# Optimization experiments

Measured on AMD Instinct MI355X. Metric: run time of the kernel, lower is better.

The kernel has to match this reference:

```python
import jax, jax.numpy as jnp
import numpy as np

B, S, D = 1, 4096, 512
QK_DIM, N_HEADS = 512, 8
HEAD_DIM = QK_DIM // N_HEADS


def setup_inputs() -> dict:
    key = jax.random.key(0)
    ks = jax.random.split(key, 9)
    s_in = 1.0 / np.sqrt(D)
    s_v = 1.0 / np.sqrt(QK_DIM)
    return {
        "x": jax.random.normal(ks[0], (B, S, D), dtype=jnp.float32),
        # torch nn.Linear convention: weight (out_features, in_features)
        "Wq": jax.random.uniform(ks[1], (QK_DIM, D), jnp.float32, -s_in, s_in),
        "bq": jax.random.uniform(ks[2], (QK_DIM,), jnp.float32, -s_in, s_in),
        "Wk": jax.random.uniform(ks[3], (QK_DIM, D), jnp.float32, -s_in, s_in),
        "bk": jax.random.uniform(ks[4], (QK_DIM,), jnp.float32, -s_in, s_in),
        "Wv": jax.random.uniform(ks[5], (QK_DIM, D), jnp.float32, -s_in, s_in),
        "bv": jax.random.uniform(ks[6], (QK_DIM,), jnp.float32, -s_in, s_in),
        "Wo": jax.random.uniform(ks[7], (D, QK_DIM), jnp.float32, -s_v, s_v),
        "bo": jax.random.uniform(ks[8], (D,), jnp.float32, -s_v, s_v),
    }


def reference(x, Wq, bq, Wk, bk, Wv, bv, Wo, bo):
    # Faithful to source: tokens flattened over batch*seq before head split.
    n = x.shape[0] * x.shape[1]  # B*S
    Q = (x @ Wq.T + bq).reshape(n, N_HEADS, HEAD_DIM).transpose(1, 0, 2)  # (H, N, hd)
    K = (x @ Wk.T + bk).reshape(n, N_HEADS, HEAD_DIM).transpose(1, 0, 2)
    V = (x @ Wv.T + bv).reshape(n, N_HEADS, HEAD_DIM).transpose(1, 0, 2)
    scores = jnp.einsum("hnd,hmd->hnm", Q, K) / np.sqrt(HEAD_DIM).astype(np.float32)
    attn = jax.nn.softmax(scores, axis=-1)                # (H, N, N) materialized
    ctx = jnp.einsum("hnm,hmd->hnd", attn, V)             # (H, N, hd)
    ctx = ctx.transpose(1, 0, 2).reshape(n, QK_DIM)       # (N, qk_dim)
    return ctx @ Wo.T + bo                                # (N, input_dim)
```

## Files before the change

### kernel.cpp

```cpp
#include <hip/hip_runtime.h>
#include <math.h>

#define N_TOK 4096
#define DMODEL 512
#define NH 8
#define HD 64

typedef __attribute__((ext_vector_type(4))) float f32x4;
typedef __attribute__((ext_vector_type(8))) _Float16 f16x8;
typedef __attribute__((ext_vector_type(4))) _Float16 f16x4;

#define MFMA16(A, B, C) __builtin_amdgcn_mfma_f32_16x16x32_f16(A, B, C, 0, 0, 0)

__global__ __launch_bounds__(256) void cast_x(const float* __restrict__ x,
                                              _Float16* __restrict__ X16) {
    int i = (blockIdx.x * 256 + threadIdx.x) * 8;
    f32x4 a = *(const f32x4*)&x[i];
    f32x4 b = *(const f32x4*)&x[i + 4];
    f16x8 o = {(_Float16)a[0], (_Float16)a[1], (_Float16)a[2], (_Float16)a[3],
               (_Float16)b[0], (_Float16)b[1], (_Float16)b[2], (_Float16)b[3]};
    *(f16x8*)&X16[i] = o;
}

__global__ __launch_bounds__(768) void qkv_gemm(const _Float16* __restrict__ X16,
                                                const float* __restrict__ Wq,
                                                const float* __restrict__ bq,
                                                const float* __restrict__ Wk,
                                                const float* __restrict__ bk,
                                                const float* __restrict__ Wv,
                                                const float* __restrict__ bv,
                                                _Float16* __restrict__ Q16,
                                                _Float16* __restrict__ K16,
                                                _Float16* __restrict__ VT16) {
    __shared__ __align__(16) _Float16 smem[46080];
    _Float16* AsB = smem;
    _Float16* WsB = smem + 18432;

    int t = threadIdx.x;
    int w = t >> 6, l = t & 63, quad = l >> 4, ln = l & 15;
    int z = w >> 2, ww = w & 3;
    int n0 = blockIdx.x * 128, o0 = blockIdx.y * 64;
    int h = o0 >> 6;

    const float* biasz = (z == 0) ? bq : (z == 1) ? bk : bv;

    f32x4 acc[2][4] = {};

    bool isA = (t < 256);
    int asr = t >> 3, asc = (t & 7) * 8;
    int tt = t - 256;
    int wr = tt >> 3, wc = (tt & 7) * 8;

    const _Float16* Abase = X16 + (size_t)n0 * DMODEL;
    const float* W0 = Wq + (size_t)o0 * DMODEL;
    const float* W1 = Wk + (size_t)o0 * DMODEL;
    const float* W2 = Wv + (size_t)o0 * DMODEL;

    f16x8 pa[4];
    f32x4 pw[3][2];
    if (isA) {
#pragma unroll
        for (int r = 0; r < 4; r++)
            pa[r] = *(const f16x8*)&Abase[(size_t)(asr + r * 32) * DMODEL + asc];
    } else {
        pw[0][0] = *(const f32x4*)&W0[(size_t)wr * DMODEL + wc];
        pw[0][1] = *(const f32x4*)&W0[(size_t)wr * DMODEL + wc + 4];
        pw[1][0] = *(const f32x4*)&W1[(size_t)wr * DMODEL + wc];
        pw[1][1] = *(const f32x4*)&W1[(size_t)wr * DMODEL + wc + 4];
        pw[2][0] = *(const f32x4*)&W2[(size_t)wr * DMODEL + wc];
        pw[2][1] = *(const f32x4*)&W2[(size_t)wr * DMODEL + wc + 4];
    }

    for (int it = 0; it < 8; it++) {
        int p = it & 1;
        if (isA) {
#pragma unroll
            for (int r = 0; r < 4; r++)
                *(f16x8*)&AsB[(size_t)(p * 128 + asr + r * 32) * 72 + asc] = pa[r];
        } else {
#pragma unroll
            for (int zt = 0; zt < 3; zt++) {
                f16x8 wv_ = {(_Float16)pw[zt][0][0], (_Float16)pw[zt][0][1],
                             (_Float16)pw[zt][0][2], (_Float16)pw[zt][0][3],
                             (_Float16)pw[zt][1][0], (_Float16)pw[zt][1][1],
                             (_Float16)pw[zt][1][2], (_Float16)pw[zt][1][3]};
                *(f16x8*)&WsB[(size_t)((p * 3 + zt) * 64 + wr) * 72 + wc] = wv_;
            }
        }
        __syncthreads();

        int k1 = (it + 1) * 64;
        if (k1 < DMODEL) {
            if (isA) {
#pragma unroll
                for (int r = 0; r < 4; r++)
                    pa[r] = *(const f16x8*)&Abase[(size_t)(asr + r * 32) * DMODEL + k1 + asc];
            } else {
                pw[0][0] = *(const f32x4*)&W0[(size_t)wr * DMODEL + k1 + wc];
                pw[0][1] = *(const f32x4*)&W0[(size_t)wr * DMODEL + k1 + wc + 4];
                pw[1][0] = *(const f32x4*)&W1[(size_t)wr * DMODEL + k1 + wc];
                pw[1][1] = *(const f32x4*)&W1[(size_t)wr * DMODEL + k1 + wc + 4];
                pw[2][0] = *(const f32x4*)&W2[(size_t)wr * DMODEL + k1 + wc];
                pw[2][1] = *(const f32x4*)&W2[(size_t)wr * DMODEL + k1 + wc + 4];
            }
        }

#pragma unroll
        for (int ks = 0; ks < 2; ks++) {
            f16x8 af0 = *(const f16x8*)&AsB[(size_t)(p * 128 + ww * 32 + ln) * 72 +
                                            ks * 32 + quad * 8];
            f16x8 af1 = *(const f16x8*)&AsB[(size_t)(p * 128 + ww * 32 + 16 + ln) * 72 +
                                            ks * 32 + quad * 8];
#pragma unroll
            for (int c = 0; c < 4; c++) {
                f16x8 bf = *(const f16x8*)&WsB[(size_t)((p * 3 + z) * 64 + c * 16 + ln) * 72 +
                                               ks * 32 + quad * 8];
                acc[0][c] = MFMA16(af0, bf, acc[0][c]);
                acc[1][c] = MFMA16(af1, bf, acc[1][c]);
            }
        }
    }

    __syncthreads();

    const float QS = 0.125f * 1.44269504088896340736f;
    _Float16* Qs = smem;
    _Float16* Ksep = smem + 9216;
    _Float16* Vt = smem + 18432;

    if (z < 2) {
        _Float16* st = (z == 0) ? Qs : Ksep;
        float sc_ = (z == 0) ? QS : 1.0f;
#pragma unroll
        for (int c = 0; c < 4; c++) {
            float bv_ = biasz[o0 + c * 16 + ln];
#pragma unroll
            for (int rt = 0; rt < 2; rt++)
#pragma unroll
                for (int i = 0; i < 4; i++) {
                    int lr = ww * 32 + rt * 16 + quad * 4 + i;
                    st[(size_t)lr * 72 + c * 16 + ln] =
                        (_Float16)((acc[rt][c][i] + bv_) * sc_);
                }
        }
    } else {
#pragma unroll
        for (int c = 0; c < 4; c++) {
            float bv_ = biasz[o0 + c * 16 + ln];
#pragma unroll
            for (int rt = 0; rt < 2; rt++)
#pragma unroll
                for (int i = 0; i < 4; i++) {
                    int np = (ww >> 1) * 64 + (ww & 1) * 32 + quad * 8 + rt * 4 + i;
                    Vt[(size_t)(c * 16 + ln) * 136 + np] = (_Float16)(acc[rt][c][i] + bv_);
                }
        }
    }
    __syncthreads();

    if (t < 256) {
#pragma unroll
        for (int k = 0; k < 4; k++) {
            int row = k * 32 + (t >> 3), col = (t & 7) * 8;
            *(f16x8*)&Q16[((size_t)h * N_TOK + n0 + row) * HD + col] =
                *(const f16x8*)&Qs[(size_t)row * 72 + col];
        }
    } else if (t < 512) {
        int u = t - 256;
#pragma unroll
        for (int k = 0; k < 4; k++) {
            int row = k * 32 + (u >> 3), col = (u & 7) * 8;
            *(f16x8*)&K16[((size_t)h * N_TOK + n0 + row) * HD + col] =
                *(const f16x8*)&Ksep[(size_t)row * 72 + col];
        }
    } else {
        int u = t - 512;
#pragma unroll
        for (int k = 0; k < 4; k++) {
            int d = k * 16 + (u >> 4), col = (u & 15) * 8;
            *(f16x8*)&VT16[((size_t)h * HD + d) * N_TOK + n0 + col] =
                *(const f16x8*)&Vt[(size_t)d * 136 + col];
        }
    }
}

#define SWZ(r, c) (((r) * 64) + ((c) ^ (((r) & 7) << 3)))

__global__ __launch_bounds__(1024) void flash_mfma(const _Float16* __restrict__ Q16,
                                                   const _Float16* __restrict__ K16,
                                                   const _Float16* __restrict__ VT16,
                                                   _Float16* __restrict__ OP,
                                                   float* __restrict__ LS) {
    __shared__ __align__(16) _Float16 Ks[2][64 * 64];
    __shared__ __align__(16) _Float16 Vs[2][64 * 64];

    int t = threadIdx.x;
    int w = t >> 6, l = t & 63, quad = l >> 4, ln = l & 15;
    int bid = blockIdx.x;
    int h = bid & 7;
    int qt = (bid >> 3) & 7;
    int s = bid >> 6;
    int q0 = qt * 512 + w * 32;
    int m_start = s * 1024;

    f16x8 qf[2][2];
#pragma unroll
    for (int rt = 0; rt < 2; rt++) {
        const _Float16* qp = &Q16[((size_t)h * N_TOK + q0 + rt * 16 + ln) * HD + quad * 8];
        qf[rt][0] = *(const f16x8*)qp;
        qf[rt][1] = *(const f16x8*)(qp + 32);
    }

    f32x4 oacc[2][4] = {};
    float lsum[2] = {0.0f, 0.0f};

    const _Float16* kbase = K16 + (size_t)h * N_TOK * HD;
    const _Float16* vbase = VT16 + (size_t)h * HD * N_TOK;
    int g = t >> 9, tt = t & 511;
    int srow = tt >> 3, scol = (tt & 7) * 8;

    f16x8 pkv;
    if (g == 0)
        pkv = *(const f16x8*)(kbase + (size_t)(m_start + srow) * HD + scol);
    else
        pkv = *(const f16x8*)(vbase + (size_t)srow * N_TOK + m_start + scol);

    for (int it = 0; it < 16; it++) {
        int m0 = m_start + it * 64;
        int p = it & 1;
        if (g == 0)
            *(f16x8*)&Ks[p][SWZ(srow, scol)] = pkv;
        else
            *(f16x8*)&Vs[p][SWZ(srow, scol)] = pkv;
        __syncthreads();

        if (it < 15) {
            int m1 = m0 + 64;
            if (g == 0)
                pkv = *(const f16x8*)(kbase + (size_t)(m1 + srow) * HD + scol);
            else
                pkv = *(const f16x8*)(vbase + (size_t)srow * N_TOK + m1 + scol);
        }

        f16x8 kb[4][2];
#pragma unroll
        for (int c = 0; c < 4; c++) {
            kb[c][0] = *(const f16x8*)&Ks[p][SWZ(c * 16 + ln, quad * 8)];
            kb[c][1] = *(const f16x8*)&Ks[p][SWZ(c * 16 + ln, 32 + quad * 8)];
        }

        f16x8 bf[2][2];
#pragma unroll
        for (int rt = 0; rt < 2; rt++) {
            f32x4 sacc[4] = {};
#pragma unroll
            for (int kk = 0; kk < 4; kk++) {
                sacc[kk] = MFMA16(kb[kk][0], qf[rt][0], sacc[kk]);
                sacc[kk] = MFMA16(kb[kk][1], qf[rt][1], sacc[kk]);
            }
            float ls0 = 0.0f;
#pragma unroll
            for (int kk = 0; kk < 4; kk++) {
                float e0 = __builtin_exp2f(sacc[kk][0]);
                float e1 = __builtin_exp2f(sacc[kk][1]);
                float e2 = __builtin_exp2f(sacc[kk][2]);
                float e3 = __builtin_exp2f(sacc[kk][3]);
                ls0 += (e0 + e1) + (e2 + e3);
                bf[rt][kk >> 1][(kk & 1) * 4 + 0] = (_Float16)e0;
                bf[rt][kk >> 1][(kk & 1) * 4 + 1] = (_Float16)e1;
                bf[rt][kk >> 1][(kk & 1) * 4 + 2] = (_Float16)e2;
                bf[rt][kk >> 1][(kk & 1) * 4 + 3] = (_Float16)e3;
            }
            lsum[rt] += ls0;
        }

#pragma unroll
        for (int c = 0; c < 4; c++) {
            f16x8 va0 = *(const f16x8*)&Vs[p][SWZ(c * 16 + ln, quad * 8)];
            f16x8 va1 = *(const f16x8*)&Vs[p][SWZ(c * 16 + ln, 32 + quad * 8)];
            oacc[0][c] = MFMA16(va0, bf[0][0], oacc[0][c]);
            oacc[0][c] = MFMA16(va1, bf[0][1], oacc[0][c]);
            oacc[1][c] = MFMA16(va0, bf[1][0], oacc[1][c]);
            oacc[1][c] = MFMA16(va1, bf[1][1], oacc[1][c]);
        }
    }

#pragma unroll
    for (int rt = 0; rt < 2; rt++) {
        lsum[rt] += __shfl_xor(lsum[rt], 16, 64);
        lsum[rt] += __shfl_xor(lsum[rt], 32, 64);
    }

    _Float16* obase = OP + (size_t)s * N_TOK * DMODEL;
#pragma unroll
    for (int rt = 0; rt < 2; rt++) {
        int r = q0 + rt * 16 + ln;
#pragma unroll
        for (int c = 0; c < 4; c++) {
            f16x4 ov = {(_Float16)oacc[rt][c][0], (_Float16)oacc[rt][c][1],
                        (_Float16)oacc[rt][c][2], (_Float16)oacc[rt][c][3]};
            *(f16x4*)&obase[(size_t)r * DMODEL + h * HD + c * 16 + quad * 4] = ov;
        }
    }
    if (l < 16) {
#pragma unroll
        for (int rt = 0; rt < 2; rt++) {
            int r = q0 + rt * 16 + ln;
            LS[((size_t)s * NH + h) * N_TOK + r] = lsum[rt];
        }
    }
}

__global__ __launch_bounds__(512) void out_gemm(const _Float16* __restrict__ OP,
                                                const float* __restrict__ LS,
                                                const float* __restrict__ Wo,
                                                const float* __restrict__ bo,
                                                float* __restrict__ out) {
    __shared__ __align__(16) _Float16 smem[27648];
    _Float16* AsB = smem;
    _Float16* WsB = smem + 18432;

    int t = threadIdx.x;
    int w = t >> 6, l = t & 63, quad = l >> 4, ln = l & 15;
    int n0 = blockIdx.x * 128, o0 = blockIdx.y * 64;
    int sr = t >> 2, sc = (t & 3) * 16;
    int wr = t >> 3, wc = (t & 7) * 8;
    const size_t PSTR = (size_t)N_TOK * DMODEL;

    f32x4 acc[4] = {};

    const float* Wbase = Wo + (size_t)o0 * DMODEL;

    f16x8 pa[4][2];
    float lt;
    f32x4 pw0, pw1;
    {
        size_t base = (size_t)(n0 + sr) * DMODEL + sc;
#pragma unroll
        for (int s_ = 0; s_ < 4; s_++) {
            pa[s_][0] = *(const f16x8*)&OP[s_ * PSTR + base];
            pa[s_][1] = *(const f16x8*)&OP[s_ * PSTR + base + 8];
        }
        const float* ls = LS + n0 + sr;
        lt = (ls[0] + ls[NH * N_TOK]) + (ls[2 * NH * N_TOK] + ls[3 * NH * N_TOK]);
        pw0 = *(const f32x4*)&Wbase[(size_t)wr * DMODEL + wc];
        pw1 = *(const f32x4*)&Wbase[(size_t)wr * DMODEL + wc + 4];
    }

    for (int it = 0; it < 8; it++) {
        int p = it & 1;
        {
            float inv = 1.0f / lt;
            f16x8 s0, s1;
#pragma unroll
            for (int j = 0; j < 8; j++) {
                s0[j] = (_Float16)(
                    ((((float)pa[0][0][j] + (float)pa[1][0][j]) +
                      ((float)pa[2][0][j] + (float)pa[3][0][j]))) * inv);
                s1[j] = (_Float16)(
                    ((((float)pa[0][1][j] + (float)pa[1][1][j]) +
                      ((float)pa[2][1][j] + (float)pa[3][1][j]))) * inv);
            }
            *(f16x8*)&AsB[(size_t)(p * 128 + sr) * 72 + sc] = s0;
            *(f16x8*)&AsB[(size_t)(p * 128 + sr) * 72 + sc + 8] = s1;
            f16x8 wv_ = {(_Float16)pw0[0], (_Float16)pw0[1], (_Float16)pw0[2],
                         (_Float16)pw0[3], (_Float16)pw1[0], (_Float16)pw1[1],
                         (_Float16)pw1[2], (_Float16)pw1[3]};
            *(f16x8*)&WsB[(size_t)(p * 64 + wr) * 72 + wc] = wv_;
        }
        __syncthreads();

        int k1 = (it + 1) * 64;
        if (k1 < DMODEL) {
            int h1 = k1 >> 6;
            size_t base = (size_t)(n0 + sr) * DMODEL + k1 + sc;
#pragma unroll
            for (int s_ = 0; s_ < 4; s_++) {
                pa[s_][0] = *(const f16x8*)&OP[s_ * PSTR + base];
                pa[s_][1] = *(const f16x8*)&OP[s_ * PSTR + base + 8];
            }
            const float* ls = LS + (size_t)h1 * N_TOK + n0 + sr;
            lt = (ls[0] + ls[NH * N_TOK]) + (ls[2 * NH * N_TOK] + ls[3 * NH * N_TOK]);
            pw0 = *(const f32x4*)&Wbase[(size_t)wr * DMODEL + k1 + wc];
            pw1 = *(const f32x4*)&Wbase[(size_t)wr * DMODEL + k1 + wc + 4];
        }

#pragma unroll
        for (int ks = 0; ks < 2; ks++) {
            f16x8 af = *(const f16x8*)&AsB[(size_t)(p * 128 + w * 16 + ln) * 72 +
                                           ks * 32 + quad * 8];
#pragma unroll
            for (int c = 0; c < 4; c++) {
                f16x8 bf = *(const f16x8*)&WsB[(size_t)(p * 64 + c * 16 + ln) * 72 +
                                               ks * 32 + quad * 8];
                acc[c] = MFMA16(af, bf, acc[c]);
            }
        }
    }

#pragma unroll
    for (int c = 0; c < 4; c++) {
        float bv_ = bo[o0 + c * 16 + ln];
#pragma unroll
        for (int i = 0; i < 4; i++) {
            int r = n0 + w * 16 + quad * 4 + i;
            out[(size_t)r * DMODEL + o0 + c * 16 + ln] = acc[c][i] + bv_;
        }
    }
}

extern "C" void kernel_launch(void* const* d_in, const int* in_sizes, int n_in,
                              void* d_out, int out_size, void* d_ws, size_t ws_size,
                              hipStream_t stream) {
    const float* x  = (const float*)d_in[0];
    const float* Wq = (const float*)d_in[1];
    const float* bq = (const float*)d_in[2];
    const float* Wk = (const float*)d_in[3];
    const float* bk = (const float*)d_in[4];
    const float* Wv = (const float*)d_in[5];
    const float* bv = (const float*)d_in[6];
    const float* Wo = (const float*)d_in[7];
    const float* bo = (const float*)d_in[8];
    float* out = (float*)d_out;

    char* ws = (char*)d_ws;
    _Float16* X16  = (_Float16*)(ws);
    _Float16* Q16  = (_Float16*)(ws + (4u << 20));
    _Float16* K16  = (_Float16*)(ws + (8u << 20));
    _Float16* VT16 = (_Float16*)(ws + (12u << 20));
    _Float16* OP   = (_Float16*)(ws + (16u << 20));
    float*    LSp  = (float*)   (ws + (32u << 20));

    cast_x<<<1024, 256, 0, stream>>>(x, X16);

    qkv_gemm<<<dim3(32, 8), 768, 0, stream>>>(X16, Wq, bq, Wk, bk, Wv, bv,
                                              Q16, K16, VT16);

    flash_mfma<<<dim3(256), 1024, 0, stream>>>(Q16, K16, VT16, OP, LSp);

    out_gemm<<<dim3(32, 8), 512, 0, stream>>>(OP, LSp, Wo, bo, out);
}
```

Before: 155.9 us.

## Fuse x cast into QKV GEMM and compute softmax row sums via MFMA

Removes the separate cast_x kernel: qkv_gemm now loads fp32 x directly and converts to fp16 when storing into shared memory, saving a launch and a round trip of the half-precision copy of x. In the flash kernel, row sums of exp scores are computed with an MFMA against a ones vector instead of scalar adds and cross-lane shuffles. V fragments are also loaded from LDS alongside K, earlier in the loop. This costs more global bytes per A load in the GEMM and extra MFMA work and registers in the attention loop.

```diff
diff --git a/kernel.cpp b/kernel.cpp
--- a/kernel.cpp
+++ b/kernel.cpp
@@ -12,17 +12,7 @@
 
 #define MFMA16(A, B, C) __builtin_amdgcn_mfma_f32_16x16x32_f16(A, B, C, 0, 0, 0)
 
-__global__ __launch_bounds__(256) void cast_x(const float* __restrict__ x,
-                                              _Float16* __restrict__ X16) {
-    int i = (blockIdx.x * 256 + threadIdx.x) * 8;
-    f32x4 a = *(const f32x4*)&x[i];
-    f32x4 b = *(const f32x4*)&x[i + 4];
-    f16x8 o = {(_Float16)a[0], (_Float16)a[1], (_Float16)a[2], (_Float16)a[3],
-               (_Float16)b[0], (_Float16)b[1], (_Float16)b[2], (_Float16)b[3]};
-    *(f16x8*)&X16[i] = o;
-}
-
-__global__ __launch_bounds__(768) void qkv_gemm(const _Float16* __restrict__ X16,
+__global__ __launch_bounds__(768) void qkv_gemm(const float* __restrict__ x,
                                                 const float* __restrict__ Wq,
                                                 const float* __restrict__ bq,
                                                 const float* __restrict__ Wk,
@@ -51,17 +41,19 @@
     int tt = t - 256;
     int wr = tt >> 3, wc = (tt & 7) * 8;
 
-    const _Float16* Abase = X16 + (size_t)n0 * DMODEL;
+    const float* Abase = x + (size_t)n0 * DMODEL;
     const float* W0 = Wq + (size_t)o0 * DMODEL;
     const float* W1 = Wk + (size_t)o0 * DMODEL;
     const float* W2 = Wv + (size_t)o0 * DMODEL;
 
-    f16x8 pa[4];
+    f32x4 pa[4][2];
     f32x4 pw[3][2];
     if (isA) {
 #pragma unroll
-        for (int r = 0; r < 4; r++)
-            pa[r] = *(const f16x8*)&Abase[(size_t)(asr + r * 32) * DMODEL + asc];
+        for (int r = 0; r < 4; r++) {
+            pa[r][0] = *(const f32x4*)&Abase[(size_t)(asr + r * 32) * DMODEL + asc];
+            pa[r][1] = *(const f32x4*)&Abase[(size_t)(asr + r * 32) * DMODEL + asc + 4];
+        }
     } else {
         pw[0][0] = *(const f32x4*)&W0[(size_t)wr * DMODEL + wc];
         pw[0][1] = *(const f32x4*)&W0[(size_t)wr * DMODEL + wc + 4];
@@ -75,8 +67,13 @@
         int p = it & 1;
         if (isA) {
 #pragma unroll
-            for (int r = 0; r < 4; r++)
-                *(f16x8*)&AsB[(size_t)(p * 128 + asr + r * 32) * 72 + asc] = pa[r];
+            for (int r = 0; r < 4; r++) {
+                f16x8 av = {(_Float16)pa[r][0][0], (_Float16)pa[r][0][1],
+                            (_Float16)pa[r][0][2], (_Float16)pa[r][0][3],
+                            (_Float16)pa[r][1][0], (_Float16)pa[r][1][1],
+                            (_Float16)pa[r][1][2], (_Float16)pa[r][1][3]};
+                *(f16x8*)&AsB[(size_t)(p * 128 + asr + r * 32) * 72 + asc] = av;
+            }
         } else {
 #pragma unroll
             for (int zt = 0; zt < 3; zt++) {
@@ -93,8 +90,10 @@
         if (k1 < DMODEL) {
             if (isA) {
 #pragma unroll
-                for (int r = 0; r < 4; r++)
-                    pa[r] = *(const f16x8*)&Abase[(size_t)(asr + r * 32) * DMODEL + k1 + asc];
+                for (int r = 0; r < 4; r++) {
+                    pa[r][0] = *(const f32x4*)&Abase[(size_t)(asr + r * 32) * DMODEL + k1 + asc];
+                    pa[r][1] = *(const f32x4*)&Abase[(size_t)(asr + r * 32) * DMODEL + k1 + asc + 4];
+                }
             } else {
                 pw[0][0] = *(const f32x4*)&W0[(size_t)wr * DMODEL + k1 + wc];
                 pw[0][1] = *(const f32x4*)&W0[(size_t)wr * DMODEL + k1 + wc + 4];
@@ -211,8 +210,12 @@
         qf[rt][1] = *(const f16x8*)(qp + 32);
     }
 
+    f16x8 ones;
+#pragma unroll
+    for (int j = 0; j < 8; j++) ones[j] = (_Float16)1.0f;
+
     f32x4 oacc[2][4] = {};
-    float lsum[2] = {0.0f, 0.0f};
+    f32x4 lacc[2] = {};
 
     const _Float16* kbase = K16 + (size_t)h * N_TOK * HD;
     const _Float16* vbase = VT16 + (size_t)h * HD * N_TOK;
@@ -242,11 +245,13 @@
                 pkv = *(const f16x8*)(vbase + (size_t)srow * N_TOK + m1 + scol);
         }
 
-        f16x8 kb[4][2];
+        f16x8 kb[4][2], vb[4][2];
 #pragma unroll
         for (int c = 0; c < 4; c++) {
             kb[c][0] = *(const f16x8*)&Ks[p][SWZ(c * 16 + ln, quad * 8)];
             kb[c][1] = *(const f16x8*)&Ks[p][SWZ(c * 16 + ln, 32 + quad * 8)];
+            vb[c][0] = *(const f16x8*)&Vs[p][SWZ(c * 16 + ln, quad * 8)];
+            vb[c][1] = *(const f16x8*)&Vs[p][SWZ(c * 16 + ln, 32 + quad * 8)];
         }
 
         f16x8 bf[2][2];
@@ -258,37 +263,28 @@
                 sacc[kk] = MFMA16(kb[kk][0], qf[rt][0], sacc[kk]);
                 sacc[kk] = MFMA16(kb[kk][1], qf[rt][1], sacc[kk]);
             }
-            float ls0 = 0.0f;
 #pragma unroll
             for (int kk = 0; kk < 4; kk++) {
-                float e0 = __builtin_exp2f(sacc[kk][0]);
-                float e1 = __builtin_exp2f(sacc[kk][1]);
-                float e2 = __builtin_exp2f(sacc[kk][2]);
-                float e3 = __builtin_exp2f(sacc[kk][3]);
-                ls0 += (e0 + e1) + (e2 + e3);
-                bf[rt][kk >> 1][(kk & 1) * 4 + 0] = (_Float16)e0;
-                bf[rt][kk >> 1][(kk & 1) * 4 + 1] = (_Float16)e1;
-                bf[rt][kk >> 1][(kk & 1) * 4 + 2] = (_Float16)e2;
-                bf[rt][kk >> 1][(kk & 1) * 4 + 3] = (_Float16)e3;
-            }
-            lsum[rt] += ls0;
+                bf[rt][kk >> 1][(kk & 1) * 4 + 0] = (_Float16)__builtin_exp2f(sacc[kk][0]);
+                bf[rt][kk >> 1][(kk & 1) * 4 + 1] = (_Float16)__builtin_exp2f(sacc[kk][1]);
+                bf[rt][kk >> 1][(kk & 1) * 4 + 2] = (_Float16)__builtin_exp2f(sacc[kk][2]);
+                bf[rt][kk >> 1][(kk & 1) * 4 + 3] = (_Float16)__builtin_exp2f(sacc[kk][3]);
+            }
+        }
+
+#pragma unroll
+        for (int rt = 0; rt < 2; rt++) {
+            lacc[rt] = MFMA16(ones, bf[rt][0], lacc[rt]);
+            lacc[rt] = MFMA16(ones, bf[rt][1], lacc[rt]);
         }
 
 #pragma unroll
         for (int c = 0; c < 4; c++) {
-            f16x8 va0 = *(const f16x8*)&Vs[p][SWZ(c * 16 + ln, quad * 8)];
-            f16x8 va1 = *(const f16x8*)&Vs[p][SWZ(c * 16 + ln, 32 + quad * 8)];
-            oacc[0][c] = MFMA16(va0, bf[0][0], oacc[0][c]);
-            oacc[0][c] = MFMA16(va1, bf[0][1], oacc[0][c]);
-            oacc[1][c] = MFMA16(va0, bf[1][0], oacc[1][c]);
-            oacc[1][c] = MFMA16(va1, bf[1][1], oacc[1][c]);
-        }
-    }
-
-#pragma unroll
-    for (int rt = 0; rt < 2; rt++) {
-        lsum[rt] += __shfl_xor(lsum[rt], 16, 64);
-        lsum[rt] += __shfl_xor(lsum[rt], 32, 64);
+            oacc[0][c] = MFMA16(vb[c][0], bf[0][0], oacc[0][c]);
+            oacc[0][c] = MFMA16(vb[c][1], bf[0][1], oacc[0][c]);
+            oacc[1][c] = MFMA16(vb[c][0], bf[1][0], oacc[1][c]);
+            oacc[1][c] = MFMA16(vb[c][1], bf[1][1], oacc[1][c]);
+        }
     }
 
     _Float16* obase = OP + (size_t)s * N_TOK * DMODEL;
@@ -306,7 +302,7 @@
 #pragma unroll
         for (int rt = 0; rt < 2; rt++) {
             int r = q0 + rt * 16 + ln;
-            LS[((size_t)s * NH + h) * N_TOK + r] = lsum[rt];
+            LS[((size_t)s * NH + h) * N_TOK + r] = lacc[rt][0];
         }
     }
 }
@@ -424,16 +420,13 @@
     float* out = (float*)d_out;
 
     char* ws = (char*)d_ws;
-    _Float16* X16  = (_Float16*)(ws);
     _Float16* Q16  = (_Float16*)(ws + (4u << 20));
     _Float16* K16  = (_Float16*)(ws + (8u << 20));
     _Float16* VT16 = (_Float16*)(ws + (12u << 20));
     _Float16* OP   = (_Float16*)(ws + (16u << 20));
     float*    LSp  = (float*)   (ws + (32u << 20));
 
-    cast_x<<<1024, 256, 0, stream>>>(x, X16);
-
-    qkv_gemm<<<dim3(32, 8), 768, 0, stream>>>(X16, Wq, bq, Wk, bk, Wv, bv,
+    qkv_gemm<<<dim3(32, 8), 768, 0, stream>>>(x, Wq, bq, Wk, bk, Wv, bv,
                                               Q16, K16, VT16);
 
     flash_mfma<<<dim3(256), 1024, 0, stream>>>(Q16, K16, VT16, OP, LSp);
```

New measurement: 152.9 us. No clear change (-1.9%).
